# Kernel tuning notes

Hardware: AMD Instinct MI355X
Metric: run time of the kernel (lower is better)

Reference implementation:

```python
import jax, jax.numpy as jnp
import numpy as np

HEAD_SIZE = 12
INNER_DIM = 64
BIG_NEG = 1e12


def _sinusoidal(seq_len, dim):
    # interleaved [sin, cos, sin, cos, ...] like SinusoidalPositionEmbedding('zero')
    pos = jnp.arange(seq_len, dtype=jnp.float32)
    inv = jnp.power(10000.0, -2.0 * jnp.arange(dim // 2, dtype=jnp.float32) / dim)
    ang = pos[:, None] * inv[None, :]                       # (L, dim/2)
    return jnp.stack([jnp.sin(ang), jnp.cos(ang)], axis=-1).reshape(seq_len, dim)


def _rope_rotate(x, cos_pos, sin_pos):
    # x: (B, L, H, D); rotate-half per interleaved RoPE
    x2 = jnp.stack([-x[..., 1::2], x[..., ::2]], axis=-1).reshape(x.shape)
    return x * cos_pos + x2 * sin_pos


def setup_inputs() -> dict:
    key = jax.random.key(0)
    k1, k2 = jax.random.split(key)
    B, L, HID = 16, 512, 768
    sequence_output = jax.random.normal(k1, (B, L, HID), dtype=jnp.float32)
    mask = jnp.ones((B, L), dtype=jnp.float32)
    W = jax.random.normal(k2, (HID, HEAD_SIZE * INNER_DIM * 2), dtype=jnp.float32) * 0.02
    b = jnp.zeros((HEAD_SIZE * INNER_DIM * 2,), dtype=jnp.float32)
    return {"sequence_output": sequence_output, "mask": mask, "W": W, "b": b}


def reference(sequence_output, mask, W, b):
    B, L, _ = sequence_output.shape
    H, D = HEAD_SIZE, INNER_DIM
    out = sequence_output @ W + b                           # (B, L, H*2D)
    out = out.reshape(B, L, H, 2 * D)
    qw, kw = out[..., :D], out[..., D:]                     # (B, L, H, D)
    pos = _sinusoidal(L, D)                                 # (L, D)
    cos_pos = jnp.repeat(pos[:, None, 1::2], 2, axis=-1)    # (L, 1, D)
    sin_pos = jnp.repeat(pos[:, None, ::2], 2, axis=-1)
    qw = _rope_rotate(qw, cos_pos, sin_pos)
    kw = _rope_rotate(kw, cos_pos, sin_pos)
    logits = jnp.einsum('bmhd,bnhd->bhmn', qw, kw)          # (B, H, L, L)
    pad = mask[:, None, None, :]                            # (B, 1, 1, L)
    logits = logits * pad - (1.0 - pad) * BIG_NEG
    tril = jnp.tril(jnp.ones((L, L), dtype=logits.dtype), -1)
    logits = logits - tril * BIG_NEG
    return logits / (D ** 0.5)
```

## Files before the change

kernel.cpp:

```cpp
#include <hip/hip_runtime.h>
#include <hip/hip_bf16.h>
#include <stdint.h>

typedef __bf16 bf16x8 __attribute__((ext_vector_type(8)));
typedef __bf16 bf16x4 __attribute__((ext_vector_type(4)));
typedef float f32x4 __attribute__((ext_vector_type(4)));

#define HEADS 12
#define DDIM 64
#define LSEQ 512
#define HID 768
#define NOUT 1536
#define BIG_NEG 1000000000000.0f

__device__ __forceinline__ void gl_lds16(const void* g, void* l) {
    __builtin_amdgcn_global_load_lds(
        (const __attribute__((address_space(1))) void*)g,
        (__attribute__((address_space(3))) void*)l, 16, 0, 0);
}

__device__ __forceinline__ void ldsbar() {
    asm volatile("s_waitcnt lgkmcnt(0)" ::: "memory");
    __builtin_amdgcn_s_barrier();
}

__global__ __launch_bounds__(256) void prep_k(
    const float* __restrict__ X, const float* __restrict__ W,
    __bf16* __restrict__ Xb, __bf16* __restrict__ Wt,
    float* __restrict__ cosT, float* __restrict__ sinT) {

    int blk = blockIdx.x;
    if (blk < 3072) {
        size_t idx = ((size_t)blk * 256 + threadIdx.x) * 8;
        float4 f0 = *(const float4*)(X + idx);
        float4 f1 = *(const float4*)(X + idx + 4);
        bf16x8 p = {(__bf16)f0.x,(__bf16)f0.y,(__bf16)f0.z,(__bf16)f0.w,
                    (__bf16)f1.x,(__bf16)f1.y,(__bf16)f1.z,(__bf16)f1.w};
        *(bf16x8*)(Xb + idx) = p;
    } else if (blk < 4224) {
        __shared__ float Ls[32][33];
        int b2 = blk - 3072;
        int n0 = (b2 % 48) * 32, k0 = (b2 / 48) * 32;
        int tx = threadIdx.x & 31, ty = threadIdx.x >> 5;
#pragma unroll
        for (int rr = 0; rr < 4; ++rr) {
            int k = ty + rr * 8;
            Ls[k][tx] = W[(size_t)(k0 + k) * NOUT + n0 + tx];
        }
        __syncthreads();
#pragma unroll
        for (int rr = 0; rr < 4; ++rr) {
            int n = ty + rr * 8;
            Wt[(size_t)(n0 + n) * HID + k0 + tx] = (__bf16)Ls[tx][n];
        }
    } else {
        int idx = (blk - 4224) * 256 + threadIdx.x;
        int l = idx >> 6, d = idx & 63;
        int p = d >> 1;
        float inv = powf(10000.0f, (-2.0f * (float)p) / 64.0f);
        float ang = (float)l * inv;
        cosT[idx] = cosf(ang);
        sinT[idx] = sinf(ang);
    }
}

__global__ __launch_bounds__(256) void proj_rope_k(
    const __bf16* __restrict__ Xb, const __bf16* __restrict__ Wt,
    const float* __restrict__ bias, const float* __restrict__ cosT,
    const float* __restrict__ sinT,
    __bf16* __restrict__ qws, __bf16* __restrict__ kws) {

    __shared__ __bf16 As[128 * 64];
    __shared__ __bf16 Bs[128 * 64];

    const int tid = threadIdx.x;
    const int m0 = blockIdx.x * 128, n0 = blockIdx.y * 128;
    const int lane = tid & 63, wid = tid >> 6;
    const int wm = wid >> 1, wn = wid & 1;
    const int lr = lane & 15, kg = lane >> 4;

    const int srow = tid >> 3;
    const int sch  = tid & 7;

    f32x4 acc[4][4] = {};

    for (int k0 = 0; k0 < HID; k0 += 64) {
#pragma unroll
        for (int j = 0; j < 4; ++j) {
            int r = j * 32 + srow;
            int cs = sch ^ (r & 7);
            gl_lds16(Wt + (size_t)(n0 + r) * HID + k0 + cs * 8,
                     (char*)Bs + j * 4096 + tid * 16);
            gl_lds16(Xb + (size_t)(m0 + r) * HID + k0 + cs * 8,
                     (char*)As + j * 4096 + tid * 16);
        }
        __syncthreads();
#pragma unroll
        for (int ks = 0; ks < 2; ++ks) {
            bf16x8 af[4], xf[4];
#pragma unroll
            for (int ai = 0; ai < 4; ++ai) {
                int row = wn * 64 + ai * 16 + lr;
                int c = (kg + ks * 4) ^ (row & 7);
                af[ai] = *(bf16x8*)((char*)Bs + row * 128 + c * 16);
            }
#pragma unroll
            for (int bi = 0; bi < 4; ++bi) {
                int row = wm * 64 + bi * 16 + lr;
                int c = (kg + ks * 4) ^ (row & 7);
                xf[bi] = *(bf16x8*)((char*)As + row * 128 + c * 16);
            }
#pragma unroll
            for (int ai = 0; ai < 4; ++ai)
#pragma unroll
                for (int bi = 0; bi < 4; ++bi)
                    acc[ai][bi] = __builtin_amdgcn_mfma_f32_16x16x32_bf16(
                        af[ai], xf[bi], acc[ai][bi], 0, 0, 0);
        }
        __syncthreads();
    }

#pragma unroll
    for (int ai = 0; ai < 4; ++ai) {
        int nb = n0 + wn * 64 + ai * 16 + kg * 4;
        int h = nb >> 7, d2 = nb & 127;
        int d = d2 & 63;
        __bf16* dst = (d2 >= 64) ? kws : qws;
        float4 b4 = *(const float4*)&bias[nb];
#pragma unroll
        for (int bi = 0; bi < 4; ++bi) {
            int m = m0 + wm * 64 + bi * 16 + lr;
            int bidx = m >> 9, lpos = m & 511;
            float4 c4 = *(const float4*)&cosT[lpos * 64 + d];
            float4 s4 = *(const float4*)&sinT[lpos * 64 + d];
            float v0 = acc[ai][bi][0] + b4.x;
            float v1 = acc[ai][bi][1] + b4.y;
            float v2 = acc[ai][bi][2] + b4.z;
            float v3 = acc[ai][bi][3] + b4.w;
            bf16x4 o;
            o[0] = (__bf16)(v0 * c4.x - v1 * s4.x);
            o[1] = (__bf16)(v1 * c4.y + v0 * s4.y);
            o[2] = (__bf16)(v2 * c4.z - v3 * s4.z);
            o[3] = (__bf16)(v3 * c4.w + v2 * s4.w);
            *(bf16x4*)&dst[(((size_t)bidx * HEADS + h) * LSEQ + lpos) * DDIM + d] = o;
        }
    }
}

__global__ __launch_bounds__(256) void attn_k(
    const __bf16* __restrict__ qws, const __bf16* __restrict__ kws,
    const float* __restrict__ mask, float* __restrict__ out) {

    __shared__ __align__(16) char smem[49664];
    __bf16* Qs = (__bf16*)smem;
    __bf16* Ks = (__bf16*)(smem + 16384);
    float*  Es = (float*)(smem + 32768);

    const int tid = threadIdx.x;
    const int bh = blockIdx.y;
    const int m0 = blockIdx.x * 128;
    const int lane = tid & 63, wid = tid >> 6;
    const int wm = wid >> 1, wn = wid & 1;
    const int lr = lane & 15, kg = lane >> 4;

    const __bf16* qbase = qws + ((size_t)bh * LSEQ + m0) * DDIM;
    const __bf16* kbase = kws + (size_t)bh * LSEQ * DDIM;

    const int row32 = tid >> 3, ch = tid & 7;
#pragma unroll
    for (int j = 0; j < 4; ++j) {
        int r = j * 32 + row32;
        int cs = ch ^ (r & 7);
        gl_lds16(qbase + (size_t)r * DDIM + cs * 8, (char*)Qs + j * 4096 + tid * 16);
        gl_lds16(kbase + (size_t)r * DDIM + cs * 8, (char*)Ks + j * 4096 + tid * 16);
    }
    __syncthreads();

    const int b = bh / HEADS;
    const int colb = (tid & 31) * 4;
    const int rrow = tid >> 5;
    float* obase = out + (size_t)bh * LSEQ * LSEQ;

    for (int nt = 0; nt < 4; ++nt) {
        f32x4 acc[4][4] = {};
#pragma unroll
        for (int ks = 0; ks < 2; ++ks) {
            bf16x8 af[4], qf[4];
#pragma unroll
            for (int ai = 0; ai < 4; ++ai) {
                int row = wn * 64 + ai * 16 + lr;
                int c = (kg + ks * 4) ^ (row & 7);
                af[ai] = *(bf16x8*)((char*)Ks + row * 128 + c * 16);
            }
#pragma unroll
            for (int bi = 0; bi < 4; ++bi) {
                int row = wm * 64 + bi * 16 + lr;
                int c = (kg + ks * 4) ^ (row & 7);
                qf[bi] = *(bf16x8*)((char*)Qs + row * 128 + c * 16);
            }
#pragma unroll
            for (int ai = 0; ai < 4; ++ai)
#pragma unroll
                for (int bi = 0; bi < 4; ++bi)
                    acc[ai][bi] = __builtin_amdgcn_mfma_f32_16x16x32_bf16(
                        af[ai], qf[bi], acc[ai][bi], 0, 0, 0);
        }
        ldsbar();

        const int n0 = nt * 128;
        const float4 p4 = *(const float4*)&mask[b * LSEQ + n0 + colb];

        if (nt < 3) {
#pragma unroll
            for (int j = 0; j < 4; ++j) {
                int r = j * 32 + row32;
                int cs = ch ^ (r & 7);
                gl_lds16(kbase + (size_t)(n0 + 128 + r) * DDIM + cs * 8,
                         (char*)Ks + j * 4096 + tid * 16);
            }
        }

#pragma unroll
        for (int p = 0; p < 4; ++p) {
            ldsbar();
            if (wm == (p >> 1)) {
                const int bi0 = (p & 1) * 2;
#pragma unroll
                for (int bb = 0; bb < 2; ++bb) {
                    int bi = bi0 + bb;
                    int row = bb * 16 + lr;
#pragma unroll
                    for (int ai = 0; ai < 4; ++ai) {
                        int n = wn * 64 + ai * 16 + kg * 4;
                        *(f32x4*)&Es[row * 132 + n] = acc[ai][bi];
                    }
                }
            }
            ldsbar();
#pragma unroll
            for (int j = 0; j < 4; ++j) {
                int rloc = rrow + j * 8;
                int m = m0 + p * 32 + rloc;
                f32x4 v = *(f32x4*)&Es[rloc * 132 + colb];
                int n = n0 + colb;
                f32x4 o;
                o[0] = (v[0] * p4.x - (1.0f - p4.x) * BIG_NEG
                        - ((m > n + 0) ? BIG_NEG : 0.0f)) * 0.125f;
                o[1] = (v[1] * p4.y - (1.0f - p4.y) * BIG_NEG
                        - ((m > n + 1) ? BIG_NEG : 0.0f)) * 0.125f;
                o[2] = (v[2] * p4.z - (1.0f - p4.z) * BIG_NEG
                        - ((m > n + 2) ? BIG_NEG : 0.0f)) * 0.125f;
                o[3] = (v[3] * p4.w - (1.0f - p4.w) * BIG_NEG
                        - ((m > n + 3) ? BIG_NEG : 0.0f)) * 0.125f;
                __builtin_nontemporal_store(o, (f32x4*)&obase[(size_t)m * LSEQ + n]);
            }
        }

        if (nt < 3) {
            asm volatile("s_waitcnt vmcnt(16) lgkmcnt(0)" ::: "memory");
            __builtin_amdgcn_s_barrier();
        }
    }
}

extern "C" void kernel_launch(void* const* d_in, const int* in_sizes, int n_in,
                              void* d_out, int out_size, void* d_ws, size_t ws_size,
                              hipStream_t stream) {
    const float* X    = (const float*)d_in[0];
    const float* mask = (const float*)d_in[1];
    const float* W    = (const float*)d_in[2];
    const float* bias = (const float*)d_in[3];
    float* out = (float*)d_out;

    char* ws = (char*)d_ws;
    float*  cosT = (float*)ws;
    float*  sinT = (float*)(ws + 131072);
    __bf16* Wt   = (__bf16*)(ws + 262144);
    __bf16* Xb   = (__bf16*)(ws + 2621440);
    __bf16* qws  = (__bf16*)(ws + 2621440 + 12582912);
    __bf16* kws  = (__bf16*)(ws + 2621440 + 2*12582912);

    prep_k<<<4352, 256, 0, stream>>>(X, W, Xb, Wt, cosT, sinT);
    proj_rope_k<<<dim3(64, 12), 256, 0, stream>>>(Xb, Wt, bias, cosT, sinT, qws, kws);
    attn_k<<<dim3(4, 192), 256, 0, stream>>>(qws, kws, mask, out);
}
```

Baseline: 94.05 us.

## Switch projection and logits GEMMs to FP8 and skip fully masked causal tiles

```diff
diff --git a/kernel.cpp b/kernel.cpp
--- a/kernel.cpp
+++ b/kernel.cpp
@@ -1,9 +1,6 @@
 #include <hip/hip_runtime.h>
-#include <hip/hip_bf16.h>
 #include <stdint.h>
 
-typedef __bf16 bf16x8 __attribute__((ext_vector_type(8)));
-typedef __bf16 bf16x4 __attribute__((ext_vector_type(4)));
 typedef float f32x4 __attribute__((ext_vector_type(4)));
 
 #define HEADS 12
@@ -24,9 +21,15 @@
     __builtin_amdgcn_s_barrier();
 }
 
+__device__ __forceinline__ uint32_t pk4_fp8(float a, float b, float c, float d) {
+    uint32_t v = __builtin_amdgcn_cvt_pk_fp8_f32(a, b, 0, false);
+    v = __builtin_amdgcn_cvt_pk_fp8_f32(c, d, v, true);
+    return v;
+}
+
 __global__ __launch_bounds__(256) void prep_k(
     const float* __restrict__ X, const float* __restrict__ W,
-    __bf16* __restrict__ Xb, __bf16* __restrict__ Wt,
+    uint8_t* __restrict__ Xq, uint8_t* __restrict__ Wtq,
     float* __restrict__ cosT, float* __restrict__ sinT) {
 
     int blk = blockIdx.x;
@@ -34,9 +37,10 @@
         size_t idx = ((size_t)blk * 256 + threadIdx.x) * 8;
         float4 f0 = *(const float4*)(X + idx);
         float4 f1 = *(const float4*)(X + idx + 4);
-        bf16x8 p = {(__bf16)f0.x,(__bf16)f0.y,(__bf16)f0.z,(__bf16)f0.w,
-                    (__bf16)f1.x,(__bf16)f1.y,(__bf16)f1.z,(__bf16)f1.w};
-        *(bf16x8*)(Xb + idx) = p;
+        uint2 p;
+        p.x = pk4_fp8(f0.x, f0.y, f0.z, f0.w);
+        p.y = pk4_fp8(f1.x, f1.y, f1.z, f1.w);
+        *(uint2*)(Xq + idx) = p;
     } else if (blk < 4224) {
         __shared__ float Ls[32][33];
         int b2 = blk - 3072;
@@ -48,11 +52,9 @@
             Ls[k][tx] = W[(size_t)(k0 + k) * NOUT + n0 + tx];
         }
         __syncthreads();
-#pragma unroll
-        for (int rr = 0; rr < 4; ++rr) {
-            int n = ty + rr * 8;
-            Wt[(size_t)(n0 + n) * HID + k0 + tx] = (__bf16)Ls[tx][n];
-        }
+        int n = threadIdx.x >> 3, c = threadIdx.x & 7;
+        uint32_t w = pk4_fp8(Ls[4*c][n], Ls[4*c+1][n], Ls[4*c+2][n], Ls[4*c+3][n]);
+        *(uint32_t*)(Wtq + (size_t)(n0 + n) * HID + k0 + c * 4) = w;
     } else {
         int idx = (blk - 4224) * 256 + threadIdx.x;
         int l = idx >> 6, d = idx & 63;
@@ -65,13 +67,13 @@
 }
 
 __global__ __launch_bounds__(256) void proj_rope_k(
-    const __bf16* __restrict__ Xb, const __bf16* __restrict__ Wt,
+    const uint8_t* __restrict__ Xq, const uint8_t* __restrict__ Wtq,
     const float* __restrict__ bias, const float* __restrict__ cosT,
     const float* __restrict__ sinT,
-    __bf16* __restrict__ qws, __bf16* __restrict__ kws) {
-
-    __shared__ __bf16 As[128 * 64];
-    __shared__ __bf16 Bs[128 * 64];
+    uint8_t* __restrict__ qq, uint8_t* __restrict__ kq) {
+
+    __shared__ __align__(16) uint8_t As[128 * 64];
+    __shared__ __align__(16) uint8_t Bs[128 * 64];
 
     const int tid = threadIdx.x;
     const int m0 = blockIdx.x * 128, n0 = blockIdx.y * 128;
@@ -79,43 +81,42 @@
     const int wm = wid >> 1, wn = wid & 1;
     const int lr = lane & 15, kg = lane >> 4;
 
-    const int srow = tid >> 3;
-    const int sch  = tid & 7;
+    const int srow = tid >> 2, sc = tid & 3;
 
     f32x4 acc[4][4] = {};
 
     for (int k0 = 0; k0 < HID; k0 += 64) {
 #pragma unroll
-        for (int j = 0; j < 4; ++j) {
-            int r = j * 32 + srow;
-            int cs = sch ^ (r & 7);
-            gl_lds16(Wt + (size_t)(n0 + r) * HID + k0 + cs * 8,
-                     (char*)Bs + j * 4096 + tid * 16);
-            gl_lds16(Xb + (size_t)(m0 + r) * HID + k0 + cs * 8,
-                     (char*)As + j * 4096 + tid * 16);
+        for (int j = 0; j < 2; ++j) {
+            int r = j * 64 + srow;
+            int cs = sc ^ ((r >> 1) & 3);
+            gl_lds16(Wtq + (size_t)(n0 + r) * HID + k0 + cs * 16,
+                     Bs + j * 4096 + tid * 16);
+            gl_lds16(Xq + (size_t)(m0 + r) * HID + k0 + cs * 16,
+                     As + j * 4096 + tid * 16);
         }
         __syncthreads();
 #pragma unroll
         for (int ks = 0; ks < 2; ++ks) {
-            bf16x8 af[4], xf[4];
+            unsigned long long af[4], xf[4];
 #pragma unroll
             for (int ai = 0; ai < 4; ++ai) {
                 int row = wn * 64 + ai * 16 + lr;
-                int c = (kg + ks * 4) ^ (row & 7);
-                af[ai] = *(bf16x8*)((char*)Bs + row * 128 + c * 16);
+                int sl = (ks * 4 + kg) ^ (row & 6);
+                af[ai] = *(const unsigned long long*)(Bs + row * 64 + sl * 8);
             }
 #pragma unroll
             for (int bi = 0; bi < 4; ++bi) {
                 int row = wm * 64 + bi * 16 + lr;
-                int c = (kg + ks * 4) ^ (row & 7);
-                xf[bi] = *(bf16x8*)((char*)As + row * 128 + c * 16);
+                int sl = (ks * 4 + kg) ^ (row & 6);
+                xf[bi] = *(const unsigned long long*)(As + row * 64 + sl * 8);
             }
 #pragma unroll
             for (int ai = 0; ai < 4; ++ai)
 #pragma unroll
                 for (int bi = 0; bi < 4; ++bi)
-                    acc[ai][bi] = __builtin_amdgcn_mfma_f32_16x16x32_bf16(
-                        af[ai], xf[bi], acc[ai][bi], 0, 0, 0);
+                    acc[ai][bi] = __builtin_amdgcn_mfma_f32_16x16x32_fp8_fp8(
+                        (long long)af[ai], (long long)xf[bi], acc[ai][bi], 0, 0, 0);
         }
         __syncthreads();
     }
@@ -125,7 +126,7 @@
         int nb = n0 + wn * 64 + ai * 16 + kg * 4;
         int h = nb >> 7, d2 = nb & 127;
         int d = d2 & 63;
-        __bf16* dst = (d2 >= 64) ? kws : qws;
+        uint8_t* dst = (d2 >= 64) ? kq : qq;
         float4 b4 = *(const float4*)&bias[nb];
 #pragma unroll
         for (int bi = 0; bi < 4; ++bi) {
@@ -137,73 +138,83 @@
             float v1 = acc[ai][bi][1] + b4.y;
             float v2 = acc[ai][bi][2] + b4.z;
             float v3 = acc[ai][bi][3] + b4.w;
-            bf16x4 o;
-            o[0] = (__bf16)(v0 * c4.x - v1 * s4.x);
-            o[1] = (__bf16)(v1 * c4.y + v0 * s4.y);
-            o[2] = (__bf16)(v2 * c4.z - v3 * s4.z);
-            o[3] = (__bf16)(v3 * c4.w + v2 * s4.w);
-            *(bf16x4*)&dst[(((size_t)bidx * HEADS + h) * LSEQ + lpos) * DDIM + d] = o;
+            float o0 = v0 * c4.x - v1 * s4.x;
+            float o1 = v1 * c4.y + v0 * s4.y;
+            float o2 = v2 * c4.z - v3 * s4.z;
+            float o3 = v3 * c4.w + v2 * s4.w;
+            uint32_t pw = pk4_fp8(o0, o1, o2, o3);
+            *(uint32_t*)(dst + (((size_t)bidx * HEADS + h) * LSEQ + lpos) * DDIM + d) = pw;
         }
     }
 }
 
 __global__ __launch_bounds__(256) void attn_k(
-    const __bf16* __restrict__ qws, const __bf16* __restrict__ kws,
+    const uint8_t* __restrict__ qq, const uint8_t* __restrict__ kq,
     const float* __restrict__ mask, float* __restrict__ out) {
 
-    __shared__ __align__(16) char smem[49664];
-    __bf16* Qs = (__bf16*)smem;
-    __bf16* Ks = (__bf16*)(smem + 16384);
-    float*  Es = (float*)(smem + 32768);
+    __shared__ __align__(16) uint8_t Qs[8192];
+    __shared__ __align__(16) uint8_t Ks[8192];
+    __shared__ __align__(16) float Es[32 * 132];
+    __shared__ int wok[4];
 
     const int tid = threadIdx.x;
     const int bh = blockIdx.y;
-    const int m0 = blockIdx.x * 128;
+    const int mtile = blockIdx.x;
+    const int m0 = mtile * 128;
     const int lane = tid & 63, wid = tid >> 6;
     const int wm = wid >> 1, wn = wid & 1;
     const int lr = lane & 15, kg = lane >> 4;
-
-    const __bf16* qbase = qws + ((size_t)bh * LSEQ + m0) * DDIM;
-    const __bf16* kbase = kws + (size_t)bh * LSEQ * DDIM;
-
-    const int row32 = tid >> 3, ch = tid & 7;
-#pragma unroll
-    for (int j = 0; j < 4; ++j) {
-        int r = j * 32 + row32;
-        int cs = ch ^ (r & 7);
-        gl_lds16(qbase + (size_t)r * DDIM + cs * 8, (char*)Qs + j * 4096 + tid * 16);
-        gl_lds16(kbase + (size_t)r * DDIM + cs * 8, (char*)Ks + j * 4096 + tid * 16);
+    const int b = bh / HEADS;
+
+    int myok = 1;
+    for (int c0 = tid; c0 < m0; c0 += 256)
+        myok &= (mask[b * LSEQ + c0] == 1.0f) ? 1 : 0;
+    unsigned long long bal = __ballot(myok);
+    if (lane == 0) wok[wid] = (bal == ~0ull) ? 1 : 0;
+    ldsbar();
+    const int nstart = (wok[0] & wok[1] & wok[2] & wok[3]) ? mtile : 0;
+
+    const uint8_t* qbase = qq + ((size_t)bh * LSEQ + m0) * DDIM;
+    const uint8_t* kbase = kq + (size_t)bh * LSEQ * DDIM;
+
+    const int srow = tid >> 2, sc = tid & 3;
+#pragma unroll
+    for (int j = 0; j < 2; ++j) {
+        int r = j * 64 + srow;
+        int cs = sc ^ ((r >> 1) & 3);
+        gl_lds16(qbase + (size_t)r * DDIM + cs * 16, Qs + j * 4096 + tid * 16);
+        gl_lds16(kbase + (size_t)(nstart * 128 + r) * DDIM + cs * 16,
+                 Ks + j * 4096 + tid * 16);
     }
     __syncthreads();
 
-    const int b = bh / HEADS;
     const int colb = (tid & 31) * 4;
     const int rrow = tid >> 5;
     float* obase = out + (size_t)bh * LSEQ * LSEQ;
 
-    for (int nt = 0; nt < 4; ++nt) {
+    for (int nt = nstart; nt < 4; ++nt) {
         f32x4 acc[4][4] = {};
 #pragma unroll
         for (int ks = 0; ks < 2; ++ks) {
-            bf16x8 af[4], qf[4];
+            unsigned long long af[4], qf[4];
 #pragma unroll
             for (int ai = 0; ai < 4; ++ai) {
                 int row = wn * 64 + ai * 16 + lr;
-                int c = (kg + ks * 4) ^ (row & 7);
-                af[ai] = *(bf16x8*)((char*)Ks + row * 128 + c * 16);
+                int sl = (ks * 4 + kg) ^ (row & 6);
+                af[ai] = *(const unsigned long long*)(Ks + row * 64 + sl * 8);
             }
 #pragma unroll
             for (int bi = 0; bi < 4; ++bi) {
                 int row = wm * 64 + bi * 16 + lr;
-                int c = (kg + ks * 4) ^ (row & 7);
-                qf[bi] = *(bf16x8*)((char*)Qs + row * 128 + c * 16);
+                int sl = (ks * 4 + kg) ^ (row & 6);
+                qf[bi] = *(const unsigned long long*)(Qs + row * 64 + sl * 8);
             }
 #pragma unroll
             for (int ai = 0; ai < 4; ++ai)
 #pragma unroll
                 for (int bi = 0; bi < 4; ++bi)
-                    acc[ai][bi] = __builtin_amdgcn_mfma_f32_16x16x32_bf16(
-                        af[ai], qf[bi], acc[ai][bi], 0, 0, 0);
+                    acc[ai][bi] = __builtin_amdgcn_mfma_f32_16x16x32_fp8_fp8(
+                        (long long)af[ai], (long long)qf[bi], acc[ai][bi], 0, 0, 0);
         }
         ldsbar();
 
@@ -212,11 +223,11 @@
 
         if (nt < 3) {
 #pragma unroll
-            for (int j = 0; j < 4; ++j) {
-                int r = j * 32 + row32;
-                int cs = ch ^ (r & 7);
-                gl_lds16(kbase + (size_t)(n0 + 128 + r) * DDIM + cs * 8,
-                         (char*)Ks + j * 4096 + tid * 16);
+            for (int j = 0; j < 2; ++j) {
+                int r = j * 64 + srow;
+                int cs = sc ^ ((r >> 1) & 3);
+                gl_lds16(kbase + (size_t)((nt + 1) * 128 + r) * DDIM + cs * 16,
+                         Ks + j * 4096 + tid * 16);
             }
         }
 
@@ -261,6 +272,19 @@
             __builtin_amdgcn_s_barrier();
         }
     }
+
+    const float CONSTV = (-BIG_NEG) * 0.125f;
+    f32x4 cv = {CONSTV, CONSTV, CONSTV, CONSTV};
+    for (int nt2 = 0; nt2 < nstart; ++nt2) {
+        int n = nt2 * 128 + colb;
+#pragma unroll
+        for (int p = 0; p < 4; ++p)
+#pragma unroll
+            for (int j = 0; j < 4; ++j) {
+                int m = m0 + p * 32 + rrow + j * 8;
+                __builtin_nontemporal_store(cv, (f32x4*)&obase[(size_t)m * LSEQ + n]);
+            }
+    }
 }
 
 extern "C" void kernel_launch(void* const* d_in, const int* in_sizes, int n_in,
@@ -273,14 +297,14 @@
     float* out = (float*)d_out;
 
     char* ws = (char*)d_ws;
-    float*  cosT = (float*)ws;
-    float*  sinT = (float*)(ws + 131072);
-    __bf16* Wt   = (__bf16*)(ws + 262144);
-    __bf16* Xb   = (__bf16*)(ws + 2621440);
-    __bf16* qws  = (__bf16*)(ws + 2621440 + 12582912);
-    __bf16* kws  = (__bf16*)(ws + 2621440 + 2*12582912);
-
-    prep_k<<<4352, 256, 0, stream>>>(X, W, Xb, Wt, cosT, sinT);
-    proj_rope_k<<<dim3(64, 12), 256, 0, stream>>>(Xb, Wt, bias, cosT, sinT, qws, kws);
-    attn_k<<<dim3(4, 192), 256, 0, stream>>>(qws, kws, mask, out);
-}
+    float*   cosT = (float*)ws;
+    float*   sinT = (float*)(ws + 131072);
+    uint8_t* Wtq  = (uint8_t*)(ws + 262144);
+    uint8_t* Xq   = (uint8_t*)(ws + 1441792);
+    uint8_t* qq   = (uint8_t*)(ws + 7733248);
+    uint8_t* kq   = (uint8_t*)(ws + 14024704);
+
+    prep_k<<<4352, 256, 0, stream>>>(X, W, Xq, Wtq, cosT, sinT);
+    proj_rope_k<<<dim3(64, 12), 256, 0, stream>>>(Xq, Wtq, bias, cosT, sinT, qq, kq);
+    attn_k<<<dim3(4, 192), 256, 0, stream>>>(qq, kq, mask, out);
+}
```

After: 86.63 us. 1.09x faster.
